# Optimization experiments

Measured on AMD Instinct MI355X. Metric: run time of the kernel, lower is better.

## Reference

```python
import jax, jax.numpy as jnp
import numpy as np

DN = ('NCHW', 'OIHW', 'NCHW')

def _conv(x, w, groups=1, padding=0):
    return jax.lax.conv_general_dilated(
        x, w, window_strides=(1, 1), padding=[(padding, padding)] * 2,
        dimension_numbers=DN, feature_group_count=groups)

def _bn(x, scale, shift):
    # precomputed inference BN: x * scale + shift, per channel (NCHW)
    return x * scale[None, :, None, None] + shift[None, :, None, None]

def _channel_shuffle(x, g):
    n, c, h, w = x.shape
    return x.reshape(n, g, c // g, h, w).transpose(0, 2, 1, 3, 4).reshape(n, c, h, w)

def setup_inputs() -> dict:
    key = jax.random.key(0)
    ks = jax.random.split(key, 13)
    N, Cin, H, W = 32, 240, 56, 56
    Cout, G = 480, 3
    mid = Cout // 4  # 120
    inp = {
        'x': jax.random.normal(ks[0], (N, Cin, H, W), jnp.float32),
        'w1': jax.random.normal(ks[1], (mid, Cin // G, 1, 1), jnp.float32) * 0.05,
        'scale1': jax.random.uniform(ks[2], (mid,), jnp.float32, 0.5, 1.5),
        'shift1': jax.random.normal(ks[3], (mid,), jnp.float32) * 0.1,
        'w2': jax.random.normal(ks[4], (mid, 1, 3, 3), jnp.float32) * 0.05,
        'scale2': jax.random.uniform(ks[5], (mid,), jnp.float32, 0.5, 1.5),
        'shift2': jax.random.normal(ks[6], (mid,), jnp.float32) * 0.1,
        'w3': jax.random.normal(ks[7], (Cout, mid // G, 1, 1), jnp.float32) * 0.05,
        'scale3': jax.random.uniform(ks[8], (Cout,), jnp.float32, 0.5, 1.5),
        'shift3': jax.random.normal(ks[9], (Cout,), jnp.float32) * 0.1,
        'wsc': jax.random.normal(ks[10], (Cout, Cin, 1, 1), jnp.float32) * 0.05,
        'scale_sc': jax.random.uniform(ks[11], (Cout,), jnp.float32, 0.5, 1.5),
        'shift_sc': jax.random.normal(ks[12], (Cout,), jnp.float32) * 0.1,
        'groups': G,
    }
    return inp

def reference(x, w1, scale1, shift1, w2, scale2, shift2, w3, scale3, shift3,
              wsc, scale_sc, shift_sc, groups):
    g = int(groups)
    mid = w1.shape[0]
    # conv1 (grouped 1x1) -> fused BN + ReLU
    y = _conv(x, w1, groups=g)
    y = jax.nn.relu(_bn(y, scale1, shift1))
    # conv2 (depthwise 3x3) -> fused BN + channel shuffle
    y = _conv(y, w2, groups=mid, padding=1)
    y = _channel_shuffle(_bn(y, scale2, shift2), g)
    # conv3 (grouped 1x1)
    y = _conv(y, w3, groups=g)
    # shortcut: 1x1 conv (in_channels != out_channels)
    z = _conv(x, wsc)
    # fused final: relu(BN3(y)) + BN_sc(z)
    return jax.nn.relu(_bn(y, scale3, shift3)) + _bn(z, scale_sc, shift_sc)
```

## Files before the change

kernel.cpp:

```cpp
#include <hip/hip_runtime.h>

typedef short bf16x8 __attribute__((ext_vector_type(8)));
typedef float f32x4 __attribute__((ext_vector_type(4)));

namespace {
constexpr int kHW = 3136;
constexpr int kNPx = 32 * kHW;
constexpr int kPtiles = kNPx / 16;
constexpr size_t kXbiShorts = (size_t)kPtiles * 4096;
}

__device__ __align__(16) unsigned short g_w1i[3 * 4 * 48 * 32];
__device__ __align__(16) unsigned short g_wsci[8 * 480 * 32];
__device__ __align__(16) unsigned short g_w3i[2 * 480 * 32];

static __device__ __forceinline__ unsigned short f2b(float f) {
  unsigned u = __float_as_uint(f);
  u = (u + 0x7fffu + ((u >> 16) & 1u)) >> 16;
  return (unsigned short)u;
}
static __device__ __forceinline__ f32x4 mfma16(bf16x8 a, bf16x8 b, f32x4 c) {
  return __builtin_amdgcn_mfma_f32_16x16x32_bf16(a, b, c, 0, 0, 0);
}
static __device__ __forceinline__ bf16x8 ldg8(const unsigned short* p) {
  return *reinterpret_cast<const bf16x8*>(p);
}

__global__ __launch_bounds__(256) void prep_weights(
    const float* __restrict__ w1, const float* __restrict__ wsc,
    const float* __restrict__ w3) {
  const int idx = blockIdx.x * 256 + threadIdx.x;
  if (idx < 18432) {
    const int g = idx / 6144, r = idx % 6144, kb = r / 1536;
    const int j = (r % 1536) / 32, k = r % 32;
    const int gk = g * 64 + kb * 32 + k;
    const int c = gk - g * 80;
    unsigned short v = 0;
    if (j < 40 && c >= 0 && c < 80) v = f2b(w1[(g * 40 + j) * 80 + c]);
    g_w1i[idx] = v;
  } else if (idx < 18432 + 122880) {
    const int i = idx - 18432;
    const int kb = i / 15360, co = (i % 15360) / 32, k = i % 32;
    const int c = kb * 32 + k;
    g_wsci[i] = (c < 240) ? f2b(wsc[co * 240 + c]) : (unsigned short)0;
  } else if (idx < 18432 + 122880 + 30720) {
    const int i = idx - 141312;
    const int kb = i / 15360, co = (i % 15360) / 32, k = i % 32;
    const int cb = co / 160;
    const int s = cb * 32 + kb * 32 + k - cb * 40;
    g_w3i[i] = (s >= 0 && s < 40) ? f2b(w3[co * 40 + s]) : (unsigned short)0;
  }
}

__global__ __launch_bounds__(256) void transpose_interleave(
    const float* __restrict__ x, unsigned short* __restrict__ xbi) {
  const int P0 = blockIdx.x * 64;
  const int px_loc = threadIdx.x >> 2, part = threadIdx.x & 3;
  const int P = P0 + px_loc;
  const int n = P / kHW, hw = P % kHW;
  const int pt = px_loc >> 4, l = px_loc & 15;
  unsigned short* dst =
      xbi + ((size_t)(P0 / 16) + pt) * 4096 + l * 32 + part * 8;
  const float* xp = x + ((size_t)n * 240) * kHW + hw;
#pragma unroll
  for (int kb = 0; kb < 8; ++kb) {
    unsigned short v[8];
#pragma unroll
    for (int j = 0; j < 8; ++j) {
      const int c = kb * 32 + part * 8 + j;
      v[j] = (c < 240) ? f2b(xp[(size_t)c * kHW]) : (unsigned short)0;
    }
    *reinterpret_cast<uint4*>(dst + kb * 512) =
        *reinterpret_cast<const uint4*>(v);
  }
}

__global__ __launch_bounds__(256) void conv1_dw_fused(
    const unsigned short* __restrict__ xbi, const float* __restrict__ scale1,
    const float* __restrict__ shift1, const float* __restrict__ w2,
    const float* __restrict__ scale2, const float* __restrict__ shift2,
    unsigned short* __restrict__ y2i) {
  const int h = blockIdx.x % 56;
  const int n = blockIdx.x / 56;
  const int A0 = (h > 0) ? (((h - 1) * 56) & ~15) : 0;

  __shared__ unsigned short lds_y1[192 * 120];
  __shared__ float lds_w2[9 * 120];
  __shared__ float lds_s2[120], lds_h2[120];

  for (int i = threadIdx.x; i < 9 * 120; i += 256) {
    const int tap = i / 120, c = i % 120;
    lds_w2[i] = w2[c * 9 + tap];
  }
  if (threadIdx.x < 120) {
    lds_s2[threadIdx.x] = scale2[threadIdx.x];
    lds_h2[threadIdx.x] = shift2[threadIdx.x];
  }

  const int lane = threadIdx.x & 63;
  const int wv = threadIdx.x >> 6;
  const int l15 = lane & 15, quad = lane >> 4;
  const size_t PT = (size_t)(n * kHW + A0) / 16 + wv * 3;

#pragma unroll
  for (int g = 0; g < 3; ++g) {
    f32x4 acc[3][3];
#pragma unroll
    for (int mt = 0; mt < 3; ++mt)
#pragma unroll
      for (int nt = 0; nt < 3; ++nt) acc[mt][nt] = (f32x4){0.f, 0.f, 0.f, 0.f};
#pragma unroll
    for (int kb = 0; kb < 4; ++kb) {
      const int kbi = 2 * g + kb;
      bf16x8 A[3];
#pragma unroll
      for (int mt = 0; mt < 3; ++mt)
        A[mt] = ldg8(xbi + (PT + mt) * 4096 + kbi * 512 + l15 * 32 + quad * 8);
#pragma unroll
      for (int nt = 0; nt < 3; ++nt) {
        const bf16x8 B = ldg8(g_w1i + (((g * 4 + kb) * 48) + nt * 16 + l15) * 32 +
                              quad * 8);
#pragma unroll
        for (int mt = 0; mt < 3; ++mt) acc[mt][nt] = mfma16(A[mt], B, acc[mt][nt]);
      }
    }
#pragma unroll
    for (int nt = 0; nt < 3; ++nt) {
      const int j = nt * 16 + l15;
      if (j < 40) {
        const int c = g * 40 + j;
        const float sc = scale1[c], sh = shift1[c];
#pragma unroll
        for (int mt = 0; mt < 3; ++mt) {
          const int pxb = wv * 48 + mt * 16 + quad * 4;
#pragma unroll
          for (int r = 0; r < 4; ++r) {
            float v = fmaf(acc[mt][nt][r], sc, sh);
            v = v > 0.f ? v : 0.f;
            lds_y1[(pxb + r) * 120 + c] = f2b(v);
          }
        }
      }
    }
  }
  __syncthreads();

  for (int idx = threadIdx.x; idx < 56 * 120; idx += 256) {
    const int c = idx % 120, w = idx / 120;
    float a = 0.f;
#pragma unroll
    for (int dy = 0; dy < 3; ++dy) {
      const int hh = h + dy - 1;
      if (hh < 0 || hh >= 56) continue;
#pragma unroll
      for (int dx = 0; dx < 3; ++dx) {
        const int ww = w + dx - 1;
        if (ww < 0 || ww >= 56) continue;
        const int pl = hh * 56 + ww - A0;
        a = fmaf(__uint_as_float((unsigned)lds_y1[pl * 120 + c] << 16),
                 lds_w2[(dy * 3 + dx) * 120 + c], a);
      }
    }
    const float v = fmaf(a, lds_s2[c], lds_h2[c]);
    const int cn = (c % 40) * 3 + c / 40;
    const int P = n * kHW + h * 56 + w;
    y2i[((size_t)(P >> 4)) * 2048 + (cn >> 5) * 512 + (P & 15) * 32 +
        (cn & 31)] = f2b(v);
  }
}

__global__ __launch_bounds__(256, 3) void conv3_sc_gemm(
    const unsigned short* __restrict__ xbi,
    const unsigned short* __restrict__ y2i, const float* __restrict__ scale3,
    const float* __restrict__ shift3, const float* __restrict__ ssc,
    const float* __restrict__ bsc, float* __restrict__ out) {
  const int pxb = blockIdx.x % 784;
  const int cb = blockIdx.x / 784;
  const int P0 = pxb * 128;
  const int lane = threadIdx.x & 63;
  const int wv = threadIdx.x >> 6;
  const int mh = wv & 1, nh = wv >> 1;
  const int l15 = lane & 15, quad = lane >> 4;
  const int cbase = cb * 160 + nh * 80;

  f32x4 acc[4][5];
#pragma unroll
  for (int mt = 0; mt < 4; ++mt)
#pragma unroll
    for (int nt = 0; nt < 5; ++nt) acc[mt][nt] = (f32x4){0.f, 0.f, 0.f, 0.f};

  const size_t PT = (size_t)(P0 / 16) + mh * 4;

#pragma unroll
  for (int kb = 0; kb < 2; ++kb) {
    const int kbi = cb + kb;
    bf16x8 A[4];
#pragma unroll
    for (int mt = 0; mt < 4; ++mt)
      A[mt] = ldg8(y2i + (PT + mt) * 2048 + kbi * 512 + l15 * 32 + quad * 8);
#pragma unroll
    for (int nt = 0; nt < 5; ++nt) {
      const bf16x8 B =
          ldg8(g_w3i + ((kb * 480) + cbase + nt * 16 + l15) * 32 + quad * 8);
#pragma unroll
      for (int mt = 0; mt < 4; ++mt) acc[mt][nt] = mfma16(A[mt], B, acc[mt][nt]);
    }
  }

#pragma unroll
  for (int nt = 0; nt < 5; ++nt) {
    const int co = cbase + nt * 16 + l15;
    const float s3 = scale3[co], h3 = shift3[co];
    const float is = 1.0f / ssc[co], h_ = bsc[co];
#pragma unroll
    for (int mt = 0; mt < 4; ++mt)
#pragma unroll
      for (int r = 0; r < 4; ++r) {
        float v3 = fmaf(acc[mt][nt][r], s3, h3);
        v3 = v3 > 0.f ? v3 : 0.f;
        acc[mt][nt][r] = (v3 + h_) * is;
      }
  }

  for (int kb = 0; kb < 8; ++kb) {
    bf16x8 A[4];
#pragma unroll
    for (int mt = 0; mt < 4; ++mt)
      A[mt] = ldg8(xbi + (PT + mt) * 4096 + kb * 512 + l15 * 32 + quad * 8);
#pragma unroll
    for (int nt = 0; nt < 5; ++nt) {
      const bf16x8 B =
          ldg8(g_wsci + ((kb * 480) + cbase + nt * 16 + l15) * 32 + quad * 8);
#pragma unroll
      for (int mt = 0; mt < 4; ++mt) acc[mt][nt] = mfma16(A[mt], B, acc[mt][nt]);
    }
  }

#pragma unroll
  for (int mt = 0; mt < 4; ++mt) {
    const int P = P0 + mh * 64 + mt * 16 + quad * 4;
    const int n = P / kHW, hw = P % kHW;
    float* ob = out + (size_t)n * 480 * kHW + hw;
#pragma unroll
    for (int nt = 0; nt < 5; ++nt) {
      const int co = cbase + nt * 16 + l15;
      const float s_ = ssc[co];
      float4 r;
      float* rp = reinterpret_cast<float*>(&r);
#pragma unroll
      for (int r4 = 0; r4 < 4; ++r4) rp[r4] = s_ * acc[mt][nt][r4];
      *reinterpret_cast<float4*>(ob + (size_t)co * kHW) = r;
    }
  }
}

extern "C" void kernel_launch(void* const* d_in, const int* in_sizes, int n_in,
                              void* d_out, int out_size, void* d_ws,
                              size_t ws_size, hipStream_t stream) {
  const float* x = (const float*)d_in[0];
  const float* w1 = (const float*)d_in[1];
  const float* scale1 = (const float*)d_in[2];
  const float* shift1 = (const float*)d_in[3];
  const float* w2 = (const float*)d_in[4];
  const float* scale2 = (const float*)d_in[5];
  const float* shift2 = (const float*)d_in[6];
  const float* w3 = (const float*)d_in[7];
  const float* scale3 = (const float*)d_in[8];
  const float* shift3 = (const float*)d_in[9];
  const float* wsc = (const float*)d_in[10];
  const float* ssc = (const float*)d_in[11];
  const float* bsc = (const float*)d_in[12];
  float* out = (float*)d_out;

  unsigned short* xbi = (unsigned short*)d_ws;
  unsigned short* y2i = xbi + kXbiShorts;

  prep_weights<<<672, 256, 0, stream>>>(w1, wsc, w3);
  transpose_interleave<<<kNPx / 64, 256, 0, stream>>>(x, xbi);
  conv1_dw_fused<<<32 * 56, 256, 0, stream>>>(xbi, scale1, shift1, w2, scale2,
                                              shift2, y2i);
  conv3_sc_gemm<<<784 * 3, 256, 0, stream>>>(xbi, y2i, scale3, shift3, ssc,
                                             bsc, out);
}
```

Before: 487.7 us.

## Split fused conv1+depthwise kernel to remove redundant halo conv1 compute

Replaces the per-row fused conv1/depthwise kernel, which recomputed conv1 for about three image rows per output row, with a standalone conv1 GEMM writing y1 to global memory and a separate vectorized depthwise+shuffle kernel. The depthwise weights are pre-scaled by scale2 in the prep kernel. This removes redundant MFMA work and the LDS-bound depthwise loop. In exchange it adds a global round trip for the intermediate activation, an extra launch, and a larger workspace.

```diff
diff --git a/kernel.cpp b/kernel.cpp
--- a/kernel.cpp
+++ b/kernel.cpp
@@ -8,17 +8,22 @@
 constexpr int kNPx = 32 * kHW;
 constexpr int kPtiles = kNPx / 16;
 constexpr size_t kXbiShorts = (size_t)kPtiles * 4096;
+constexpr size_t kY2iShorts = (size_t)kPtiles * 2048;
 }
 
 __device__ __align__(16) unsigned short g_w1i[3 * 4 * 48 * 32];
 __device__ __align__(16) unsigned short g_wsci[8 * 480 * 32];
 __device__ __align__(16) unsigned short g_w3i[2 * 480 * 32];
+__device__ __align__(16) float g_w2f[9 * 120];
 
 static __device__ __forceinline__ unsigned short f2b(float f) {
   unsigned u = __float_as_uint(f);
   u = (u + 0x7fffu + ((u >> 16) & 1u)) >> 16;
   return (unsigned short)u;
 }
+static __device__ __forceinline__ float b2f(unsigned short u) {
+  return __uint_as_float((unsigned)u << 16);
+}
 static __device__ __forceinline__ f32x4 mfma16(bf16x8 a, bf16x8 b, f32x4 c) {
   return __builtin_amdgcn_mfma_f32_16x16x32_bf16(a, b, c, 0, 0, 0);
 }
@@ -28,7 +33,8 @@
 
 __global__ __launch_bounds__(256) void prep_weights(
     const float* __restrict__ w1, const float* __restrict__ wsc,
-    const float* __restrict__ w3) {
+    const float* __restrict__ w3, const float* __restrict__ w2,
+    const float* __restrict__ scale2) {
   const int idx = blockIdx.x * 256 + threadIdx.x;
   if (idx < 18432) {
     const int g = idx / 6144, r = idx % 6144, kb = r / 1536;
@@ -49,6 +55,10 @@
     const int cb = co / 160;
     const int s = cb * 32 + kb * 32 + k - cb * 40;
     g_w3i[i] = (s >= 0 && s < 40) ? f2b(w3[co * 40 + s]) : (unsigned short)0;
+  } else if (idx < 18432 + 122880 + 30720 + 1080) {
+    const int i = idx - 172032;
+    const int tap = i / 120, c = i % 120;
+    g_w2f[i] = w2[c * 9 + tap] * scale2[c];
   }
 }
 
@@ -75,53 +85,34 @@
   }
 }
 
-__global__ __launch_bounds__(256) void conv1_dw_fused(
+__global__ __launch_bounds__(256) void conv1_gemm(
     const unsigned short* __restrict__ xbi, const float* __restrict__ scale1,
-    const float* __restrict__ shift1, const float* __restrict__ w2,
-    const float* __restrict__ scale2, const float* __restrict__ shift2,
-    unsigned short* __restrict__ y2i) {
-  const int h = blockIdx.x % 56;
-  const int n = blockIdx.x / 56;
-  const int A0 = (h > 0) ? (((h - 1) * 56) & ~15) : 0;
-
-  __shared__ unsigned short lds_y1[192 * 120];
-  __shared__ float lds_w2[9 * 120];
-  __shared__ float lds_s2[120], lds_h2[120];
-
-  for (int i = threadIdx.x; i < 9 * 120; i += 256) {
-    const int tap = i / 120, c = i % 120;
-    lds_w2[i] = w2[c * 9 + tap];
-  }
-  if (threadIdx.x < 120) {
-    lds_s2[threadIdx.x] = scale2[threadIdx.x];
-    lds_h2[threadIdx.x] = shift2[threadIdx.x];
-  }
-
+    const float* __restrict__ shift1, unsigned short* __restrict__ y1) {
   const int lane = threadIdx.x & 63;
   const int wv = threadIdx.x >> 6;
   const int l15 = lane & 15, quad = lane >> 4;
-  const size_t PT = (size_t)(n * kHW + A0) / 16 + wv * 3;
+  const size_t PT = (size_t)blockIdx.x * 8 + wv * 2;
 
 #pragma unroll
   for (int g = 0; g < 3; ++g) {
-    f32x4 acc[3][3];
-#pragma unroll
-    for (int mt = 0; mt < 3; ++mt)
+    f32x4 acc[2][3];
+#pragma unroll
+    for (int mt = 0; mt < 2; ++mt)
 #pragma unroll
       for (int nt = 0; nt < 3; ++nt) acc[mt][nt] = (f32x4){0.f, 0.f, 0.f, 0.f};
 #pragma unroll
     for (int kb = 0; kb < 4; ++kb) {
       const int kbi = 2 * g + kb;
-      bf16x8 A[3];
-#pragma unroll
-      for (int mt = 0; mt < 3; ++mt)
+      bf16x8 A[2];
+#pragma unroll
+      for (int mt = 0; mt < 2; ++mt)
         A[mt] = ldg8(xbi + (PT + mt) * 4096 + kbi * 512 + l15 * 32 + quad * 8);
 #pragma unroll
       for (int nt = 0; nt < 3; ++nt) {
         const bf16x8 B = ldg8(g_w1i + (((g * 4 + kb) * 48) + nt * 16 + l15) * 32 +
                               quad * 8);
 #pragma unroll
-        for (int mt = 0; mt < 3; ++mt) acc[mt][nt] = mfma16(A[mt], B, acc[mt][nt]);
+        for (int mt = 0; mt < 2; ++mt) acc[mt][nt] = mfma16(A[mt], B, acc[mt][nt]);
       }
     }
 #pragma unroll
@@ -131,41 +122,62 @@
         const int c = g * 40 + j;
         const float sc = scale1[c], sh = shift1[c];
 #pragma unroll
-        for (int mt = 0; mt < 3; ++mt) {
-          const int pxb = wv * 48 + mt * 16 + quad * 4;
+        for (int mt = 0; mt < 2; ++mt) {
+          const size_t pxb = (PT + mt) * 16 + quad * 4;
 #pragma unroll
           for (int r = 0; r < 4; ++r) {
             float v = fmaf(acc[mt][nt][r], sc, sh);
             v = v > 0.f ? v : 0.f;
-            lds_y1[(pxb + r) * 120 + c] = f2b(v);
+            y1[(pxb + r) * 120 + c] = f2b(v);
           }
         }
       }
     }
   }
-  __syncthreads();
-
-  for (int idx = threadIdx.x; idx < 56 * 120; idx += 256) {
-    const int c = idx % 120, w = idx / 120;
-    float a = 0.f;
-#pragma unroll
-    for (int dy = 0; dy < 3; ++dy) {
-      const int hh = h + dy - 1;
-      if (hh < 0 || hh >= 56) continue;
-#pragma unroll
-      for (int dx = 0; dx < 3; ++dx) {
-        const int ww = w + dx - 1;
-        if (ww < 0 || ww >= 56) continue;
-        const int pl = hh * 56 + ww - A0;
-        a = fmaf(__uint_as_float((unsigned)lds_y1[pl * 120 + c] << 16),
-                 lds_w2[(dy * 3 + dx) * 120 + c], a);
-      }
-    }
-    const float v = fmaf(a, lds_s2[c], lds_h2[c]);
+}
+
+__global__ __launch_bounds__(256) void dw_shuffle(
+    const unsigned short* __restrict__ y1, const float* __restrict__ shift2,
+    unsigned short* __restrict__ y2i) {
+  const int idx = blockIdx.x * 256 + threadIdx.x;
+  const int px = idx / 15, m = idx % 15;
+  const int c0 = m * 8;
+  const int n = px / kHW, hw = px % kHW;
+  const int h = hw / 56, w = hw % 56;
+
+  float acc[8];
+  {
+    const float4 s0 = *reinterpret_cast<const float4*>(shift2 + c0);
+    const float4 s1 = *reinterpret_cast<const float4*>(shift2 + c0 + 4);
+    acc[0] = s0.x; acc[1] = s0.y; acc[2] = s0.z; acc[3] = s0.w;
+    acc[4] = s1.x; acc[5] = s1.y; acc[6] = s1.z; acc[7] = s1.w;
+  }
+  const unsigned short* yb = y1 + (size_t)n * kHW * 120 + c0;
+#pragma unroll
+  for (int dy = 0; dy < 3; ++dy) {
+    const int hh = h + dy - 1;
+    if (hh < 0 || hh >= 56) continue;
+#pragma unroll
+    for (int dx = 0; dx < 3; ++dx) {
+      const int ww = w + dx - 1;
+      if (ww < 0 || ww >= 56) continue;
+      const bf16x8 v = ldg8(yb + (size_t)(hh * 56 + ww) * 120);
+      const float* wp = g_w2f + (dy * 3 + dx) * 120 + c0;
+      float wv_[8];
+      *reinterpret_cast<float4*>(wv_) = *reinterpret_cast<const float4*>(wp);
+      *reinterpret_cast<float4*>(wv_ + 4) =
+          *reinterpret_cast<const float4*>(wp + 4);
+#pragma unroll
+      for (int j = 0; j < 8; ++j)
+        acc[j] = fmaf(b2f((unsigned short)v[j]), wv_[j], acc[j]);
+    }
+  }
+  const size_t base = ((size_t)(px >> 4)) * 2048 + (px & 15) * 32;
+#pragma unroll
+  for (int j = 0; j < 8; ++j) {
+    const int c = c0 + j;
     const int cn = (c % 40) * 3 + c / 40;
-    const int P = n * kHW + h * 56 + w;
-    y2i[((size_t)(P >> 4)) * 2048 + (cn >> 5) * 512 + (P & 15) * 32 +
-        (cn & 31)] = f2b(v);
+    y2i[base + (cn >> 5) * 512 + (cn & 31)] = f2b(acc[j]);
   }
 }
 
@@ -274,11 +286,12 @@
 
   unsigned short* xbi = (unsigned short*)d_ws;
   unsigned short* y2i = xbi + kXbiShorts;
-
-  prep_weights<<<672, 256, 0, stream>>>(w1, wsc, w3);
+  unsigned short* y1 = y2i + kY2iShorts;
+
+  prep_weights<<<677, 256, 0, stream>>>(w1, wsc, w3, w2, scale2);
   transpose_interleave<<<kNPx / 64, 256, 0, stream>>>(x, xbi);
-  conv1_dw_fused<<<32 * 56, 256, 0, stream>>>(xbi, scale1, shift1, w2, scale2,
-                                              shift2, y2i);
+  conv1_gemm<<<kPtiles / 8, 256, 0, stream>>>(xbi, scale1, shift1, y1);
+  dw_shuffle<<<kNPx * 15 / 256, 256, 0, stream>>>(y1, shift2, y2i);
   conv3_sc_gemm<<<784 * 3, 256, 0, stream>>>(xbi, y2i, scale3, shift3, ssc,
                                              bsc, out);
 }
```

Result: faster. 461.8 us (-5.3%).
